# Kernel tuning notes

Measured on AMD Instinct MI355X. Metric: run time of the kernel, lower is better.

Reference implementation:

```python
import jax, jax.numpy as jnp
import numpy as np

TAU = 2.0         # LIFNode default tau
VTH = 1.0         # v_threshold
ALPHA = 2.0       # ATan surrogate alpha
TIME_STEP = 4     # hard-coded in RecurrentLIFNode
NUM_LAYERS = 4
HIDDEN = 512
INPUT = 512
T, B = 128, 512

@jax.custom_vjp
def atan_spike(x):
    # heaviside forward, ATan surrogate backward (spikingjelly surrogate.ATan)
    return (x >= 0.0).astype(x.dtype)

def _atan_fwd(x):
    return atan_spike(x), x

def _atan_bwd(x, g):
    return (g * (ALPHA / 2.0) / (1.0 + (jnp.pi / 2.0 * ALPHA * x) ** 2),)

atan_spike.defvjp(_atan_fwd, _atan_bwd)

def lif_burst(v, inp):
    # run one LIFCell time_step times with fixed input `inp`, accumulate averages
    acc_v = jnp.zeros_like(v)
    acc_s = jnp.zeros_like(v)
    for _ in range(TIME_STEP):
        v = v + (inp - v) / TAU          # neuronal_charge (decay_input=True, v_reset=None)
        s = atan_spike(v - VTH)          # neuronal_fire
        v = v - s * VTH                  # soft reset (v_reset=None)
        acc_v = acc_v + v
        acc_s = acc_s + s
    return v, acc_v / TIME_STEP, acc_s / TIME_STEP


def setup_inputs() -> dict:
    key = jax.random.key(0)
    k1, k2, k3 = jax.random.split(key, 3)
    x = jax.random.normal(k1, (T, B, INPUT), dtype=jnp.float32)
    bound = 1.0 / np.sqrt(INPUT)
    W = jax.random.uniform(k2, (HIDDEN, INPUT), dtype=jnp.float32, minval=-bound, maxval=bound)
    b = jax.random.uniform(k3, (HIDDEN,), dtype=jnp.float32, minval=-bound, maxval=bound)
    return {"x": x, "W": W, "b": b}


def reference(x, W, b):
    # x: [T, B, input]; project once (linear_ih)
    xp = jnp.einsum('tbi,hi->tbh', x, W) + b   # [T, B, H]
    Bsz, H = x.shape[1], W.shape[0]
    init_state = jnp.zeros((NUM_LAYERS, Bsz, H), dtype=x.dtype)  # current_state persists across t

    def step(cur, xt):
        curs = [cur[i] for i in range(NUM_LAYERS)]
        y = xt
        new_vs = []
        last_spk = None
        for i in range(NUM_LAYERS):
            curs[i], avg_v, avg_s = lif_burst(curs[i], y)
            new_vs.append(avg_v)
            y = avg_v          # next layer consumes averaged membrane state
            last_spk = avg_s
        return jnp.stack(curs), (last_spk, jnp.stack(new_vs))

    _, (out, states_seq) = jax.lax.scan(step, init_state, xp)
    # out: [T, B, H] averaged spikes of last layer; final new_states_list: [L, B, H]
    return out, states_seq[-1]
```

## Files before the change

kernel.cpp:

```cpp
#include <hip/hip_runtime.h>
#include <stdint.h>

#define TT 128
#define BSZ 512
#define HID 512
#define KDIM 512
#define BH (BSZ*HID)

__global__ __launch_bounds__(256) void gemm_f32(
    const float* __restrict__ A, const float* __restrict__ W, float* __restrict__ C) {
  __shared__ float As[16][132];
  __shared__ float Bs[16][132];
  const int t  = threadIdx.x;
  const int m0 = blockIdx.y * 128;
  const int n0 = blockIdx.x * 128;
  const int tx = t & 15;
  const int ty = t >> 4;

  float acc[8][8];
  #pragma unroll
  for (int i = 0; i < 8; ++i)
    #pragma unroll
    for (int j = 0; j < 8; ++j) acc[i][j] = 0.f;

  const int r0 = t >> 2;
  const int kg = t & 3;

  for (int k0 = 0; k0 < KDIM; k0 += 16) {
    const float4 a0 = *(const float4*)&A[(size_t)(m0 + r0)      * KDIM + k0 + kg*4];
    const float4 w0 = *(const float4*)&W[(size_t)(n0 + r0)      * KDIM + k0 + kg*4];
    const float4 a1 = *(const float4*)&A[(size_t)(m0 + r0 + 64) * KDIM + k0 + kg*4];
    const float4 w1 = *(const float4*)&W[(size_t)(n0 + r0 + 64) * KDIM + k0 + kg*4];
    __syncthreads();
    As[kg*4+0][r0] = a0.x; As[kg*4+1][r0] = a0.y; As[kg*4+2][r0] = a0.z; As[kg*4+3][r0] = a0.w;
    Bs[kg*4+0][r0] = w0.x; Bs[kg*4+1][r0] = w0.y; Bs[kg*4+2][r0] = w0.z; Bs[kg*4+3][r0] = w0.w;
    As[kg*4+0][r0+64] = a1.x; As[kg*4+1][r0+64] = a1.y; As[kg*4+2][r0+64] = a1.z; As[kg*4+3][r0+64] = a1.w;
    Bs[kg*4+0][r0+64] = w1.x; Bs[kg*4+1][r0+64] = w1.y; Bs[kg*4+2][r0+64] = w1.z; Bs[kg*4+3][r0+64] = w1.w;
    __syncthreads();

    #pragma unroll
    for (int kk = 0; kk < 16; ++kk) {
      const float4 xa0 = *(const float4*)&As[kk][ty*8];
      const float4 xa1 = *(const float4*)&As[kk][ty*8+4];
      const float4 xb0 = *(const float4*)&Bs[kk][tx*8];
      const float4 xb1 = *(const float4*)&Bs[kk][tx*8+4];
      const float a[8] = {xa0.x,xa0.y,xa0.z,xa0.w,xa1.x,xa1.y,xa1.z,xa1.w};
      const float b[8] = {xb0.x,xb0.y,xb0.z,xb0.w,xb1.x,xb1.y,xb1.z,xb1.w};
      #pragma unroll
      for (int i = 0; i < 8; ++i)
        #pragma unroll
        for (int j = 0; j < 8; ++j)
          acc[i][j] = __builtin_fmaf(a[i], b[j], acc[i][j]);
    }
  }

  #pragma unroll
  for (int i = 0; i < 8; ++i) {
    float4 v0 = {acc[i][0], acc[i][1], acc[i][2], acc[i][3]};
    float4 v1 = {acc[i][4], acc[i][5], acc[i][6], acc[i][7]};
    float* cp = C + (size_t)(m0 + ty*8 + i) * HID + n0 + tx*8;
    *(float4*)cp = v0;
    *(float4*)(cp + 4) = v1;
  }
}

__global__ __launch_bounds__(256) void lif_scan(
    const float* __restrict__ xp, const float* __restrict__ bias,
    float* __restrict__ outp, float* __restrict__ vstate,
    int tc, int first, int last) {
  const int idx = blockIdx.x * 256 + threadIdx.x;
  const float bh = bias[idx & (HID - 1)];
  float v[4];
  if (first) {
    #pragma unroll
    for (int l = 0; l < 4; ++l) v[l] = 0.f;
  } else {
    #pragma unroll
    for (int l = 0; l < 4; ++l) v[l] = vstate[(size_t)l * BH + idx];
  }
  float av[4] = {0.f, 0.f, 0.f, 0.f};
  const float* p = xp + idx;
  float* op = outp + idx;
  for (int t = 0; t < tc; ++t) {
    float y = p[0] + bh;
    float as3 = 0.f;
    #pragma unroll
    for (int l = 0; l < 4; ++l) {
      float vv = v[l];
      float accv = 0.f, accs = 0.f;
      #pragma unroll
      for (int k = 0; k < 4; ++k) {
        const float d = y - vv;
        vv = __builtin_fmaf(d, 0.5f, vv);
        const float spk = (vv >= 1.0f) ? 1.0f : 0.0f;
        vv -= spk;
        accv += vv;
        accs += spk;
      }
      v[l] = vv;
      const float a = accv * 0.25f;
      av[l] = a;
      y = a;
      as3 = accs;
    }
    *op = as3 * 0.25f;
    p += BH; op += BH;
  }
  if (last) {
    #pragma unroll
    for (int l = 0; l < 4; ++l) vstate[(size_t)l * BH + idx] = av[l];
  } else {
    #pragma unroll
    for (int l = 0; l < 4; ++l) vstate[(size_t)l * BH + idx] = v[l];
  }
}

extern "C" void kernel_launch(void* const* d_in, const int* in_sizes, int n_in,
                              void* d_out, int out_size, void* d_ws, size_t ws_size,
                              hipStream_t stream) {
  const float* x = (const float*)d_in[0];
  const float* W = (const float*)d_in[1];
  const float* b = (const float*)d_in[2];
  float* out    = (float*)d_out;
  float* states = out + (size_t)TT * BH;

  int tc = TT;
  while (tc > 1 && (size_t)tc * BH * 4ull > ws_size) tc >>= 1;
  float* xp = (float*)d_ws;
  const int nc = TT / tc;

  for (int c = 0; c < nc; ++c) {
    hipLaunchKernelGGL(gemm_f32, dim3(HID / 128, tc * BSZ / 128), dim3(256), 0, stream,
                       x + (size_t)c * tc * BH, W, xp);
    hipLaunchKernelGGL(lif_scan, dim3(BH / 256), dim3(256), 0, stream,
                       xp, b, out + (size_t)c * tc * BH, states,
                       tc, c == 0 ? 1 : 0, c == nc - 1 ? 1 : 0);
  }
}
```

Measured before the change: 671.6 us.

## Prefetch GEMM tiles into registers, fuse bias, and prefetch scan inputs

```diff
diff --git a/kernel.cpp b/kernel.cpp
--- a/kernel.cpp
+++ b/kernel.cpp
@@ -8,7 +8,8 @@
 #define BH (BSZ*HID)
 
 __global__ __launch_bounds__(256) void gemm_f32(
-    const float* __restrict__ A, const float* __restrict__ W, float* __restrict__ C) {
+    const float* __restrict__ A, const float* __restrict__ W,
+    const float* __restrict__ bias, float* __restrict__ C) {
   __shared__ float As[16][132];
   __shared__ float Bs[16][132];
   const int t  = threadIdx.x;
@@ -16,6 +17,8 @@
   const int n0 = blockIdx.x * 128;
   const int tx = t & 15;
   const int ty = t >> 4;
+  const int r0 = t >> 2;
+  const int kg = t & 3;
 
   float acc[8][8];
   #pragma unroll
@@ -23,27 +26,35 @@
     #pragma unroll
     for (int j = 0; j < 8; ++j) acc[i][j] = 0.f;
 
-  const int r0 = t >> 2;
-  const int kg = t & 3;
+  const float* Ap = A + (size_t)(m0 + r0) * KDIM + kg * 4;
+  const float* Wp = W + (size_t)(n0 + r0) * KDIM + kg * 4;
+
+  float4 a0 = *(const float4*)Ap;
+  float4 w0 = *(const float4*)Wp;
+  float4 a1 = *(const float4*)(Ap + (size_t)64 * KDIM);
+  float4 w1 = *(const float4*)(Wp + (size_t)64 * KDIM);
 
   for (int k0 = 0; k0 < KDIM; k0 += 16) {
-    const float4 a0 = *(const float4*)&A[(size_t)(m0 + r0)      * KDIM + k0 + kg*4];
-    const float4 w0 = *(const float4*)&W[(size_t)(n0 + r0)      * KDIM + k0 + kg*4];
-    const float4 a1 = *(const float4*)&A[(size_t)(m0 + r0 + 64) * KDIM + k0 + kg*4];
-    const float4 w1 = *(const float4*)&W[(size_t)(n0 + r0 + 64) * KDIM + k0 + kg*4];
     __syncthreads();
-    As[kg*4+0][r0] = a0.x; As[kg*4+1][r0] = a0.y; As[kg*4+2][r0] = a0.z; As[kg*4+3][r0] = a0.w;
-    Bs[kg*4+0][r0] = w0.x; Bs[kg*4+1][r0] = w0.y; Bs[kg*4+2][r0] = w0.z; Bs[kg*4+3][r0] = w0.w;
+    As[kg*4+0][r0]    = a0.x; As[kg*4+1][r0]    = a0.y; As[kg*4+2][r0]    = a0.z; As[kg*4+3][r0]    = a0.w;
+    Bs[kg*4+0][r0]    = w0.x; Bs[kg*4+1][r0]    = w0.y; Bs[kg*4+2][r0]    = w0.z; Bs[kg*4+3][r0]    = w0.w;
     As[kg*4+0][r0+64] = a1.x; As[kg*4+1][r0+64] = a1.y; As[kg*4+2][r0+64] = a1.z; As[kg*4+3][r0+64] = a1.w;
     Bs[kg*4+0][r0+64] = w1.x; Bs[kg*4+1][r0+64] = w1.y; Bs[kg*4+2][r0+64] = w1.z; Bs[kg*4+3][r0+64] = w1.w;
     __syncthreads();
 
+    if (k0 + 16 < KDIM) {
+      a0 = *(const float4*)(Ap + k0 + 16);
+      w0 = *(const float4*)(Wp + k0 + 16);
+      a1 = *(const float4*)(Ap + (size_t)64 * KDIM + k0 + 16);
+      w1 = *(const float4*)(Wp + (size_t)64 * KDIM + k0 + 16);
+    }
+
     #pragma unroll
     for (int kk = 0; kk < 16; ++kk) {
       const float4 xa0 = *(const float4*)&As[kk][ty*8];
-      const float4 xa1 = *(const float4*)&As[kk][ty*8+4];
-      const float4 xb0 = *(const float4*)&Bs[kk][tx*8];
-      const float4 xb1 = *(const float4*)&Bs[kk][tx*8+4];
+      const float4 xa1 = *(const float4*)&As[kk][ty*8 + 4];
+      const float4 xb0 = *(const float4*)&Bs[kk][tx*4];
+      const float4 xb1 = *(const float4*)&Bs[kk][64 + tx*4];
       const float a[8] = {xa0.x,xa0.y,xa0.z,xa0.w,xa1.x,xa1.y,xa1.z,xa1.w};
       const float b[8] = {xb0.x,xb0.y,xb0.z,xb0.w,xb1.x,xb1.y,xb1.z,xb1.w};
       #pragma unroll
@@ -54,22 +65,46 @@
     }
   }
 
+  const float4 bv0 = *(const float4*)&bias[n0 + tx*4];
+  const float4 bv1 = *(const float4*)&bias[n0 + 64 + tx*4];
   #pragma unroll
   for (int i = 0; i < 8; ++i) {
-    float4 v0 = {acc[i][0], acc[i][1], acc[i][2], acc[i][3]};
-    float4 v1 = {acc[i][4], acc[i][5], acc[i][6], acc[i][7]};
-    float* cp = C + (size_t)(m0 + ty*8 + i) * HID + n0 + tx*8;
-    *(float4*)cp = v0;
-    *(float4*)(cp + 4) = v1;
+    const float4 v0 = {acc[i][0] + bv0.x, acc[i][1] + bv0.y, acc[i][2] + bv0.z, acc[i][3] + bv0.w};
+    const float4 v1 = {acc[i][4] + bv1.x, acc[i][5] + bv1.y, acc[i][6] + bv1.z, acc[i][7] + bv1.w};
+    float* cp = C + (size_t)(m0 + ty*8 + i) * HID + n0;
+    *(float4*)(cp + tx*4)      = v0;
+    *(float4*)(cp + 64 + tx*4) = v1;
   }
 }
 
+__device__ __forceinline__ float lif_step(float y, float v[4], float av[4]) {
+  float as3 = 0.f;
+  #pragma unroll
+  for (int l = 0; l < 4; ++l) {
+    float vv = v[l];
+    float accv = 0.f, accs = 0.f;
+    #pragma unroll
+    for (int k = 0; k < 4; ++k) {
+      const float d = y - vv;
+      vv = __builtin_fmaf(d, 0.5f, vv);
+      const float spk = (vv >= 1.0f) ? 1.0f : 0.0f;
+      vv -= spk;
+      accv += vv;
+      accs += spk;
+    }
+    v[l] = vv;
+    const float a = accv * 0.25f;
+    av[l] = a;
+    y = a;
+    as3 = accs;
+  }
+  return as3;
+}
+
 __global__ __launch_bounds__(256) void lif_scan(
-    const float* __restrict__ xp, const float* __restrict__ bias,
-    float* __restrict__ outp, float* __restrict__ vstate,
+    const float* __restrict__ xp, float* __restrict__ outp, float* __restrict__ vstate,
     int tc, int first, int last) {
   const int idx = blockIdx.x * 256 + threadIdx.x;
-  const float bh = bias[idx & (HID - 1)];
   float v[4];
   if (first) {
     #pragma unroll
@@ -81,31 +116,17 @@
   float av[4] = {0.f, 0.f, 0.f, 0.f};
   const float* p = xp + idx;
   float* op = outp + idx;
-  for (int t = 0; t < tc; ++t) {
-    float y = p[0] + bh;
-    float as3 = 0.f;
-    #pragma unroll
-    for (int l = 0; l < 4; ++l) {
-      float vv = v[l];
-      float accv = 0.f, accs = 0.f;
-      #pragma unroll
-      for (int k = 0; k < 4; ++k) {
-        const float d = y - vv;
-        vv = __builtin_fmaf(d, 0.5f, vv);
-        const float spk = (vv >= 1.0f) ? 1.0f : 0.0f;
-        vv -= spk;
-        accv += vv;
-        accs += spk;
-      }
-      v[l] = vv;
-      const float a = accv * 0.25f;
-      av[l] = a;
-      y = a;
-      as3 = accs;
-    }
+
+  float cur = *p;
+  for (int t = 0; t < tc - 1; ++t) {
+    const float nxt = p[BH];
+    const float as3 = lif_step(cur, v, av);
     *op = as3 * 0.25f;
-    p += BH; op += BH;
+    cur = nxt; p += BH; op += BH;
   }
+  const float as3 = lif_step(cur, v, av);
+  *op = as3 * 0.25f;
+
   if (last) {
     #pragma unroll
     for (int l = 0; l < 4; ++l) vstate[(size_t)l * BH + idx] = av[l];
@@ -131,9 +152,9 @@
 
   for (int c = 0; c < nc; ++c) {
     hipLaunchKernelGGL(gemm_f32, dim3(HID / 128, tc * BSZ / 128), dim3(256), 0, stream,
-                       x + (size_t)c * tc * BH, W, xp);
+                       x + (size_t)c * tc * BH, W, b, xp);
     hipLaunchKernelGGL(lif_scan, dim3(BH / 256), dim3(256), 0, stream,
-                       xp, b, out + (size_t)c * tc * BH, states,
+                       xp, out + (size_t)c * tc * BH, states,
                        tc, c == 0 ? 1 : 0, c == nc - 1 ? 1 : 0);
   }
 }
```

Result: faster. 645.0 us (-4.0%).
